# Kernel tuning notes

Measured on AMD Instinct MI355X. Metric: run time of the kernel, lower is better.

The kernel has to match this reference:

```python
import jax, jax.numpy as jnp
import numpy as np

B, T = 64, 2000
Q_DIM, MEM_DIM, ATT_DIM = 1024, 512, 128
N_FILTERS, KERNEL = 32, 31


def setup_inputs() -> dict:
    key = jax.random.key(0)
    ks = jax.random.split(key, 8)
    s = lambda fan_in: 1.0 / np.sqrt(fan_in)
    return {
        "attention_hidden_state": jax.random.normal(ks[0], (B, Q_DIM), jnp.float32),
        "memory": jax.random.normal(ks[1], (B, T, MEM_DIM), jnp.float32),
        "attention_weights_cat": jax.random.uniform(ks[2], (B, 2, T), jnp.float32),
        "W_query": jax.random.normal(ks[3], (Q_DIM, ATT_DIM), jnp.float32) * s(Q_DIM),
        "W_memory": jax.random.normal(ks[4], (MEM_DIM, ATT_DIM), jnp.float32) * s(MEM_DIM),
        "W_v": jax.random.normal(ks[5], (ATT_DIM, 1), jnp.float32) * s(ATT_DIM),
        "W_conv": jax.random.normal(ks[6], (KERNEL, 2, N_FILTERS), jnp.float32) * s(KERNEL * 2),  # WIO layout
        "W_loc": jax.random.normal(ks[7], (N_FILTERS, ATT_DIM), jnp.float32) * s(N_FILTERS),
    }


def reference(attention_hidden_state, memory, attention_weights_cat,
              W_query, W_memory, W_v, W_conv, W_loc):
    # processed query: [B, 1, D]
    pq = jnp.tanh(attention_hidden_state @ W_query)[:, None, :]
    # processed memory: [B, T, D]
    pm = jnp.tanh(jnp.einsum('btm,md->btd', memory, W_memory))
    # location features: Conv1D 'same', no bias, channels-last input [B, T, 2]
    awc = jnp.transpose(attention_weights_cat, (0, 2, 1))
    conv = jax.lax.conv_general_dilated(
        awc, W_conv, window_strides=(1,), padding='SAME',
        dimension_numbers=('NWC', 'WIO', 'NWC'))  # [B, T, F]
    ploc = jnp.tanh(conv @ W_loc)  # [B, T, D]
    # energies: [B, T]
    energies = jnp.squeeze(jnp.tanh(pq + ploc + pm) @ W_v, -1)
    attention_weights = jax.nn.softmax(energies, axis=1)  # [B, T]
    attention_context = jnp.einsum('bt,btm->bm', attention_weights, memory)
    return attention_context, attention_weights
```

## Files before the change

### kernel.cpp

```cpp
#include <hip/hip_runtime.h>
#include <hip/hip_bf16.h>

typedef __attribute__((ext_vector_type(8))) short s16x8;
typedef __attribute__((ext_vector_type(4))) float f32x4;

#define B_SZ 64
#define T_SZ 2000
#define QD 1024
#define MD 512
#define AD 128
#define NF 32
#define KW 31
#define NTILE 63
#define ASTRIDE 1056

__device__ __forceinline__ unsigned short f2bf(float f) {
    unsigned int u = __float_as_uint(f);
    unsigned int r = (u + 0x7FFFu + ((u >> 16) & 1u)) >> 16;
    return (unsigned short)r;
}
__device__ __forceinline__ unsigned int pack2bf_manual(float a, float b) {
    return (unsigned int)f2bf(a) | ((unsigned int)f2bf(b) << 16);
}
__device__ __forceinline__ unsigned int pack2bf(float a, float b) {
    union { __hip_bfloat162 h; unsigned int u; } cv;
    cv.h = __float22bfloat162_rn(float2{a, b});
    return cv.u;
}
__device__ __forceinline__ float fast_tanh(float x) {
    float ax = fabsf(x);
    float e = __expf(2.0f * ax);
    float r = 1.0f - 2.0f * __builtin_amdgcn_rcpf(e + 1.0f);
    return x < 0.0f ? -r : r;
}

__global__ __launch_bounds__(512) void prep_kernel(
    const float* __restrict__ ahs, const float* __restrict__ Wq,
    const float* __restrict__ Wm, const float* __restrict__ Wl,
    float* __restrict__ pq, unsigned short* __restrict__ WB,
    unsigned short* __restrict__ WL) {
    const int blk = blockIdx.x, tid = threadIdx.x;
    if (blk < 64) {
        __shared__ float q_sm[QD];
        __shared__ float part[3][AD];
        ((float2*)q_sm)[tid] = ((const float2*)(ahs + blk * QD))[tid];
        __syncthreads();
        const int d = tid & 127, kh = tid >> 7;
        const int k0 = kh * 256;
        float a0 = 0, a1 = 0, a2 = 0, a3 = 0;
        #pragma unroll 4
        for (int k = k0; k < k0 + 256; k += 4) {
            a0 += q_sm[k]     * Wq[(k)     * AD + d];
            a1 += q_sm[k + 1] * Wq[(k + 1) * AD + d];
            a2 += q_sm[k + 2] * Wq[(k + 2) * AD + d];
            a3 += q_sm[k + 3] * Wq[(k + 3) * AD + d];
        }
        float s = (a0 + a1) + (a2 + a3);
        if (kh) part[kh - 1][d] = s;
        __syncthreads();
        if (tid < AD)
            pq[blk * AD + tid] =
                fast_tanh((s + part[0][tid]) + (part[1][tid] + part[2][tid]));
    } else if (blk < 80) {
        int cidx = (blk - 64) * 512 + tid;
        int n = cidx >> 10, s = (cidx >> 6) & 15, l = cidx & 63;
        int col = n * 16 + (l & 15);
        int krow = s * 32 + (l >> 4) * 8;
        float v[8];
        #pragma unroll
        for (int j = 0; j < 8; ++j) v[j] = Wm[(krow + j) * AD + col];
        uint4 pk;
        pk.x = pack2bf(v[0], v[1]); pk.y = pack2bf(v[2], v[3]);
        pk.z = pack2bf(v[4], v[5]); pk.w = pack2bf(v[6], v[7]);
        *(uint4*)(WB + cidx * 8) = pk;
    } else {
        int cidx = tid;
        int n = cidx >> 6, l = cidx & 63;
        int col = n * 16 + (l & 15);
        int krow = (l >> 4) * 8;
        float v[8];
        #pragma unroll
        for (int j = 0; j < 8; ++j) v[j] = Wl[(krow + j) * AD + col];
        uint4 pk;
        pk.x = pack2bf_manual(v[0], v[1]); pk.y = pack2bf_manual(v[2], v[3]);
        pk.z = pack2bf_manual(v[4], v[5]); pk.w = pack2bf_manual(v[6], v[7]);
        *(uint4*)(WL + cidx * 8) = pk;
    }
}

__global__ __launch_bounds__(256, 4) void energy_kernel(
    const float* __restrict__ memory, const float* __restrict__ awcat,
    const float* __restrict__ Wconv, const float* __restrict__ Wv,
    const float* __restrict__ pq, const unsigned short* __restrict__ WB,
    const unsigned short* __restrict__ WL, float* __restrict__ wts,
    float* __restrict__ ctile, float* __restrict__ mloc,
    float* __restrict__ Stile) {
    const int tile = blockIdx.x;
    const int b = blockIdx.y;
    const int t0 = tile * 32;
    const int tid = threadIdx.x;

    __shared__ __align__(16) unsigned short Atile[32 * (ASTRIDE / 2)];
    __shared__ float aw_sm[2][64];
    __shared__ __align__(16) unsigned short conv_sm[32 * 40];
    __shared__ float e_part[32][4];
    __shared__ float p_sm[32];

    float4 v[16];
    {
        const float4* msrc = (const float4*)(memory + ((size_t)b * T_SZ + t0) * MD);
        const bool full = (t0 + 32 <= T_SZ);
        if (full) {
            #pragma unroll
            for (int it = 0; it < 8; ++it) {
                int cid = it * 256 + tid;
                int r = cid >> 6, cc = cid & 63;
                v[2 * it]     = msrc[r * 128 + cc * 2];
                v[2 * it + 1] = msrc[r * 128 + cc * 2 + 1];
            }
        } else {
            #pragma unroll
            for (int it = 0; it < 8; ++it) {
                int cid = it * 256 + tid;
                int r = cid >> 6, cc = cid & 63;
                float4 z = {0, 0, 0, 0};
                bool ok = (t0 + r < T_SZ);
                v[2 * it]     = ok ? msrc[r * 128 + cc * 2]     : z;
                v[2 * it + 1] = ok ? msrc[r * 128 + cc * 2 + 1] : z;
            }
        }
    }

    if (tid < 128) {
        int c = tid >> 6, i = tid & 63;
        float val = 0.0f;
        int tv = t0 - 15 + i;
        if (i < 63 && tv >= 0 && tv < T_SZ) val = awcat[(b * 2 + c) * T_SZ + tv];
        aw_sm[c][i] = val;
    }

    {
        #pragma unroll
        for (int it = 0; it < 8; ++it) {
            int cid = it * 256 + tid;
            int r = cid >> 6, cc = cid & 63;
            float4 v0 = v[2 * it], v1 = v[2 * it + 1];
            uint4 pk;
            pk.x = pack2bf(v0.x, v0.y); pk.y = pack2bf(v0.z, v0.w);
            pk.z = pack2bf(v1.x, v1.y); pk.w = pack2bf(v1.z, v1.w);
            int off = r * ASTRIDE + ((cc * 16) ^ ((r & 7) << 4));
            *(uint4*)((char*)Atile + off) = pk;
        }
    }
    __syncthreads();

    {
        int f = tid & 31, tq = tid >> 5;
        float acc[4] = {0, 0, 0, 0};
        for (int k = 0; k < KW; ++k) {
            #pragma unroll
            for (int c = 0; c < 2; ++c) {
                float wv = Wconv[(k * 2 + c) * NF + f];
                #pragma unroll
                for (int tt = 0; tt < 4; ++tt)
                    acc[tt] += wv * aw_sm[c][tq + tt * 8 + k];
            }
        }
        #pragma unroll
        for (int tt = 0; tt < 4; ++tt)
            conv_sm[(tq + tt * 8) * 40 + f] = f2bf(acc[tt]);
    }
    __syncthreads();

    const int w = tid >> 6, l = tid & 63;
    const int lr = l & 15, lg = l >> 4;
    const int d0 = (2 * w + 0) * 16 + lr;
    const int d1 = (2 * w + 1) * 16 + lr;
    const float pqv0 = pq[b * AD + d0], pqv1 = pq[b * AD + d1];
    const float wvv0 = Wv[d0], wvv1 = Wv[d1];

    f32x4 zero4 = {0, 0, 0, 0};
    f32x4 p00 = zero4, p01 = zero4, p10 = zero4, p11 = zero4;

    const s16x8* wbp = (const s16x8*)WB;
    const int swz = (lr & 7) << 4;
    const int rbase0 = lr * ASTRIDE;
    const int rbase1 = (16 + lr) * ASTRIDE;
    const int inb = lg * 16;

    #pragma unroll
    for (int s = 0; s < 16; ++s) {
        int j = (inb + s * 64) ^ swz;
        s16x8 a0 = *(const s16x8*)((const char*)Atile + rbase0 + j);
        s16x8 a1 = *(const s16x8*)((const char*)Atile + rbase1 + j);
        s16x8 b0 = wbp[((2 * w + 0) * 16 + s) * 64 + l];
        s16x8 b1 = wbp[((2 * w + 1) * 16 + s) * 64 + l];
        p00 = __builtin_amdgcn_mfma_f32_16x16x32_bf16(a0, b0, p00, 0, 0, 0);
        p01 = __builtin_amdgcn_mfma_f32_16x16x32_bf16(a0, b1, p01, 0, 0, 0);
        p10 = __builtin_amdgcn_mfma_f32_16x16x32_bf16(a1, b0, p10, 0, 0, 0);
        p11 = __builtin_amdgcn_mfma_f32_16x16x32_bf16(a1, b1, p11, 0, 0, 0);
    }

    s16x8 la0 = *(const s16x8*)((const char*)conv_sm + (lr * 80 + lg * 16));
    s16x8 la1 = *(const s16x8*)((const char*)conv_sm + ((16 + lr) * 80 + lg * 16));
    const s16x8* wlp = (const s16x8*)WL;
    s16x8 lb0 = wlp[(2 * w + 0) * 64 + l];
    s16x8 lb1 = wlp[(2 * w + 1) * 64 + l];
    f32x4 q00 = __builtin_amdgcn_mfma_f32_16x16x32_bf16(la0, lb0, zero4, 0, 0, 0);
    f32x4 q01 = __builtin_amdgcn_mfma_f32_16x16x32_bf16(la0, lb1, zero4, 0, 0, 0);
    f32x4 q10 = __builtin_amdgcn_mfma_f32_16x16x32_bf16(la1, lb0, zero4, 0, 0, 0);
    f32x4 q11 = __builtin_amdgcn_mfma_f32_16x16x32_bf16(la1, lb1, zero4, 0, 0, 0);

    float vr[8];
    #pragma unroll
    for (int r = 0; r < 4; ++r) {
        vr[r]     = fast_tanh(pqv0 + fast_tanh(q00[r]) + fast_tanh(p00[r])) * wvv0
                  + fast_tanh(pqv1 + fast_tanh(q01[r]) + fast_tanh(p01[r])) * wvv1;
        vr[4 + r] = fast_tanh(pqv0 + fast_tanh(q10[r]) + fast_tanh(p10[r])) * wvv0
                  + fast_tanh(pqv1 + fast_tanh(q11[r]) + fast_tanh(p11[r])) * wvv1;
    }
    #pragma unroll
    for (int j = 0; j < 8; ++j) {
        float vv = vr[j];
        vv += __shfl_xor(vv, 1);
        vv += __shfl_xor(vv, 2);
        vv += __shfl_xor(vv, 4);
        vv += __shfl_xor(vv, 8);
        if (lr == 0) e_part[(j >> 2) * 16 + lg * 4 + (j & 3)][w] = vv;
    }
    __syncthreads();

    if (tid < 32) {
        int t = t0 + tid;
        bool valid = t < T_SZ;
        float e = (e_part[tid][0] + e_part[tid][1]) + (e_part[tid][2] + e_part[tid][3]);
        float m = valid ? e : -3.4e38f;
        m = fmaxf(m, __shfl_xor(m, 1));
        m = fmaxf(m, __shfl_xor(m, 2));
        m = fmaxf(m, __shfl_xor(m, 4));
        m = fmaxf(m, __shfl_xor(m, 8));
        m = fmaxf(m, __shfl_xor(m, 16));
        float p = valid ? __expf(e - m) : 0.0f;
        p_sm[tid] = p;
        float S = p;
        S += __shfl_xor(S, 1);
        S += __shfl_xor(S, 2);
        S += __shfl_xor(S, 4);
        S += __shfl_xor(S, 8);
        S += __shfl_xor(S, 16);
        if (valid) wts[b * T_SZ + t] = p;
        if (tid == 0) { mloc[b * NTILE + tile] = m; Stile[b * NTILE + tile] = S; }
    }
    __syncthreads();

    {
        float c0 = 0.0f, c1 = 0.0f;
        const int boff = tid * 4;
        #pragma unroll
        for (int t = 0; t < 32; ++t) {
            float p = p_sm[t];
            unsigned int pk = *(const unsigned int*)(
                (const char*)Atile + t * ASTRIDE + (boff ^ ((t & 7) << 4)));
            c0 += p * __uint_as_float(pk << 16);
            c1 += p * __uint_as_float(pk & 0xffff0000u);
        }
        float2 o; o.x = c0; o.y = c1;
        ((float2*)ctile)[((b * NTILE + tile) << 8) + tid] = o;
    }
}

__global__ __launch_bounds__(256) void finalize_kernel(
    const float* __restrict__ mloc, const float* __restrict__ Stile,
    const float* __restrict__ ctile, float* __restrict__ wts,
    float* __restrict__ ctx) {
    const int b = blockIdx.x, h = blockIdx.y, tid = threadIdx.x;
    __shared__ float sc_sm[NTILE + 1];
    if (tid < 64) {
        float m = (tid < NTILE) ? mloc[b * NTILE + tid] : -3.4e38f;
        float s = (tid < NTILE) ? Stile[b * NTILE + tid] : 0.0f;
        float M = m;
        M = fmaxf(M, __shfl_xor(M, 1));  M = fmaxf(M, __shfl_xor(M, 2));
        M = fmaxf(M, __shfl_xor(M, 4));  M = fmaxf(M, __shfl_xor(M, 8));
        M = fmaxf(M, __shfl_xor(M, 16)); M = fmaxf(M, __shfl_xor(M, 32));
        float e = __expf(m - M);
        float z = e * s;
        z += __shfl_xor(z, 1);  z += __shfl_xor(z, 2);
        z += __shfl_xor(z, 4);  z += __shfl_xor(z, 8);
        z += __shfl_xor(z, 16); z += __shfl_xor(z, 32);
        if (tid < NTILE) sc_sm[tid] = e / z;
    }
    __syncthreads();

    if (h == 0) {
        #pragma unroll
        for (int i = 0; i < 8; ++i) {
            int idx = tid + i * 256;
            if (idx < T_SZ) wts[b * T_SZ + idx] *= sc_sm[idx >> 5];
        }
    }

    float a = 0.0f;
    const float* cb = ctile + ((size_t)b * NTILE << 9) + h * 256 + tid;
    #pragma unroll 7
    for (int tl = 0; tl < NTILE; ++tl) a += sc_sm[tl] * cb[(size_t)tl << 9];
    ctx[b * MD + h * 256 + tid] = a;
}

extern "C" void kernel_launch(void* const* d_in, const int* in_sizes, int n_in,
                              void* d_out, int out_size, void* d_ws, size_t ws_size,
                              hipStream_t stream) {
    const float* ahs    = (const float*)d_in[0];
    const float* memory = (const float*)d_in[1];
    const float* awcat  = (const float*)d_in[2];
    const float* Wq     = (const float*)d_in[3];
    const float* Wm     = (const float*)d_in[4];
    const float* Wv     = (const float*)d_in[5];
    const float* Wconv  = (const float*)d_in[6];
    const float* Wl     = (const float*)d_in[7];

    float* out = (float*)d_out;
    float* ctx = out;
    float* wts = out + B_SZ * MD;

    char* ws = (char*)d_ws;
    float* pq             = (float*)(ws);
    unsigned short* WB    = (unsigned short*)(ws + 32768);
    unsigned short* WL    = (unsigned short*)(ws + 163840);
    float* mloc           = (float*)(ws + 172032);
    float* Stile          = (float*)(ws + 188160);
    float* ctile          = (float*)(ws + 204800);

    prep_kernel<<<81, 512, 0, stream>>>(ahs, Wq, Wm, Wl, pq, WB, WL);
    energy_kernel<<<dim3(NTILE, B_SZ), 256, 0, stream>>>(
        memory, awcat, Wconv, Wv, pq, WB, WL, wts, ctile, mloc, Stile);
    finalize_kernel<<<dim3(B_SZ, 2), 256, 0, stream>>>(mloc, Stile, ctile, wts, ctx);
}
```

Baseline: 90.54 us.

## Process four tiles per block with register prefetch of the next tile's memory

The energy kernel now loops over four consecutive 32-step tiles per block instead of launching one block per tile, which shrinks the grid from 63 to 16 blocks along T. While the current tile runs its conv, MFMA and context stages, it issues loads into registers for the first half of the next tile's memory rows. This is meant to hide global-load latency behind compute and to amortize the per-block loads of pq and Wv. In exchange it raises register pressure under launch bounds of 4 blocks per CU, which risks spills. It also reduces the number of independent blocks that can hide latency, and adds an extra barrier per tile.

```diff
diff --git a/kernel.cpp b/kernel.cpp
--- a/kernel.cpp
+++ b/kernel.cpp
@@ -88,71 +88,85 @@
     }
 }
 
-__global__ __launch_bounds__(256, 4) void energy_kernel(
+__device__ __forceinline__ void prefetch_half(
+    const float* memory, int b, int tile, int tid, float4 (&v)[8]) {
+    const float4* msrc = (const float4*)(memory + ((size_t)b * T_SZ + tile * 32) * MD);
+    #pragma unroll
+    for (int it = 0; it < 4; ++it) {
+        int cid = it * 256 + tid;
+        int r = cid >> 6, cc = cid & 63;
+        v[2 * it]     = msrc[r * 128 + cc * 2];
+        v[2 * it + 1] = msrc[r * 128 + cc * 2 + 1];
+    }
+}
+
+__device__ __forceinline__ void tile_body(
+    int b, int tile, int tid,
     const float* __restrict__ memory, const float* __restrict__ awcat,
-    const float* __restrict__ Wconv, const float* __restrict__ Wv,
-    const float* __restrict__ pq, const unsigned short* __restrict__ WB,
-    const unsigned short* __restrict__ WL, float* __restrict__ wts,
-    float* __restrict__ ctile, float* __restrict__ mloc,
-    float* __restrict__ Stile) {
-    const int tile = blockIdx.x;
-    const int b = blockIdx.y;
+    const float* __restrict__ Wconv,
+    const unsigned short* __restrict__ WB, const unsigned short* __restrict__ WL,
+    float pqv0, float pqv1, float wvv0, float wvv1,
+    float* __restrict__ wts, float* __restrict__ ctile,
+    float* __restrict__ mloc, float* __restrict__ Stile,
+    unsigned short* Atile, float (*aw_sm)[64], unsigned short* conv_sm,
+    float (*e_part)[4], float* p_sm,
+    float4 (&vin)[8], float4 (&vnext)[8], bool doPref) {
     const int t0 = tile * 32;
-    const int tid = threadIdx.x;
-
-    __shared__ __align__(16) unsigned short Atile[32 * (ASTRIDE / 2)];
-    __shared__ float aw_sm[2][64];
-    __shared__ __align__(16) unsigned short conv_sm[32 * 40];
-    __shared__ float e_part[32][4];
-    __shared__ float p_sm[32];
-
-    float4 v[16];
-    {
-        const float4* msrc = (const float4*)(memory + ((size_t)b * T_SZ + t0) * MD);
-        const bool full = (t0 + 32 <= T_SZ);
-        if (full) {
-            #pragma unroll
-            for (int it = 0; it < 8; ++it) {
-                int cid = it * 256 + tid;
-                int r = cid >> 6, cc = cid & 63;
-                v[2 * it]     = msrc[r * 128 + cc * 2];
-                v[2 * it + 1] = msrc[r * 128 + cc * 2 + 1];
-            }
-        } else {
-            #pragma unroll
-            for (int it = 0; it < 8; ++it) {
-                int cid = it * 256 + tid;
-                int r = cid >> 6, cc = cid & 63;
-                float4 z = {0, 0, 0, 0};
-                bool ok = (t0 + r < T_SZ);
-                v[2 * it]     = ok ? msrc[r * 128 + cc * 2]     : z;
-                v[2 * it + 1] = ok ? msrc[r * 128 + cc * 2 + 1] : z;
-            }
-        }
-    }
-
+    const float4* msrc = (const float4*)(memory + ((size_t)b * T_SZ + t0) * MD);
+    char* Ac = (char*)Atile;
+
+    float4 v2[8];
+    if (t0 + 32 <= T_SZ) {
+        #pragma unroll
+        for (int it = 0; it < 4; ++it) {
+            int cid = it * 256 + tid;
+            int r = 16 + (cid >> 6), cc = cid & 63;
+            v2[2 * it]     = msrc[r * 128 + cc * 2];
+            v2[2 * it + 1] = msrc[r * 128 + cc * 2 + 1];
+        }
+    } else {
+        #pragma unroll
+        for (int it = 0; it < 4; ++it) {
+            int cid = it * 256 + tid;
+            int r = 16 + (cid >> 6), cc = cid & 63;
+            float4 z = {0, 0, 0, 0};
+            bool ok = (t0 + r) < T_SZ;
+            v2[2 * it]     = ok ? msrc[r * 128 + cc * 2]     : z;
+            v2[2 * it + 1] = ok ? msrc[r * 128 + cc * 2 + 1] : z;
+        }
+    }
+
+    float awv = 0.0f;
+    const int awc_c = tid >> 6, awc_i = tid & 63;
     if (tid < 128) {
-        int c = tid >> 6, i = tid & 63;
-        float val = 0.0f;
-        int tv = t0 - 15 + i;
-        if (i < 63 && tv >= 0 && tv < T_SZ) val = awcat[(b * 2 + c) * T_SZ + tv];
-        aw_sm[c][i] = val;
-    }
-
-    {
-        #pragma unroll
-        for (int it = 0; it < 8; ++it) {
-            int cid = it * 256 + tid;
-            int r = cid >> 6, cc = cid & 63;
-            float4 v0 = v[2 * it], v1 = v[2 * it + 1];
-            uint4 pk;
-            pk.x = pack2bf(v0.x, v0.y); pk.y = pack2bf(v0.z, v0.w);
-            pk.z = pack2bf(v1.x, v1.y); pk.w = pack2bf(v1.z, v1.w);
-            int off = r * ASTRIDE + ((cc * 16) ^ ((r & 7) << 4));
-            *(uint4*)((char*)Atile + off) = pk;
-        }
-    }
-    __syncthreads();
+        int tv = t0 - 15 + awc_i;
+        if (awc_i < 63 && tv >= 0 && tv < T_SZ) awv = awcat[(b * 2 + awc_c) * T_SZ + tv];
+    }
+
+    #pragma unroll
+    for (int it = 0; it < 4; ++it) {
+        int cid = it * 256 + tid;
+        int r = cid >> 6, cc = cid & 63;
+        float4 a0 = vin[2 * it], a1 = vin[2 * it + 1];
+        uint4 pk;
+        pk.x = pack2bf(a0.x, a0.y); pk.y = pack2bf(a0.z, a0.w);
+        pk.z = pack2bf(a1.x, a1.y); pk.w = pack2bf(a1.z, a1.w);
+        *(uint4*)(Ac + r * ASTRIDE + ((cc * 16) ^ ((r & 7) << 4))) = pk;
+    }
+    #pragma unroll
+    for (int it = 0; it < 4; ++it) {
+        int cid = it * 256 + tid;
+        int r = 16 + (cid >> 6), cc = cid & 63;
+        float4 a0 = v2[2 * it], a1 = v2[2 * it + 1];
+        uint4 pk;
+        pk.x = pack2bf(a0.x, a0.y); pk.y = pack2bf(a0.z, a0.w);
+        pk.z = pack2bf(a1.x, a1.y); pk.w = pack2bf(a1.z, a1.w);
+        *(uint4*)(Ac + r * ASTRIDE + ((cc * 16) ^ ((r & 7) << 4))) = pk;
+    }
+    if (tid < 128) aw_sm[awc_c][awc_i] = awv;
+    __syncthreads();
+
+    if (doPref) prefetch_half(memory, b, tile + 1, tid, vnext);
 
     {
         int f = tid & 31, tq = tid >> 5;
@@ -174,10 +188,6 @@
 
     const int w = tid >> 6, l = tid & 63;
     const int lr = l & 15, lg = l >> 4;
-    const int d0 = (2 * w + 0) * 16 + lr;
-    const int d1 = (2 * w + 1) * 16 + lr;
-    const float pqv0 = pq[b * AD + d0], pqv1 = pq[b * AD + d1];
-    const float wvv0 = Wv[d0], wvv1 = Wv[d1];
 
     f32x4 zero4 = {0, 0, 0, 0};
     f32x4 p00 = zero4, p01 = zero4, p10 = zero4, p11 = zero4;
@@ -191,8 +201,8 @@
     #pragma unroll
     for (int s = 0; s < 16; ++s) {
         int j = (inb + s * 64) ^ swz;
-        s16x8 a0 = *(const s16x8*)((const char*)Atile + rbase0 + j);
-        s16x8 a1 = *(const s16x8*)((const char*)Atile + rbase1 + j);
+        s16x8 a0 = *(const s16x8*)(Ac + rbase0 + j);
+        s16x8 a1 = *(const s16x8*)(Ac + rbase1 + j);
         s16x8 b0 = wbp[((2 * w + 0) * 16 + s) * 64 + l];
         s16x8 b1 = wbp[((2 * w + 1) * 16 + s) * 64 + l];
         p00 = __builtin_amdgcn_mfma_f32_16x16x32_bf16(a0, b0, p00, 0, 0, 0);
@@ -260,13 +270,59 @@
         for (int t = 0; t < 32; ++t) {
             float p = p_sm[t];
             unsigned int pk = *(const unsigned int*)(
-                (const char*)Atile + t * ASTRIDE + (boff ^ ((t & 7) << 4)));
+                Ac + t * ASTRIDE + (boff ^ ((t & 7) << 4)));
             c0 += p * __uint_as_float(pk << 16);
             c1 += p * __uint_as_float(pk & 0xffff0000u);
         }
         float2 o; o.x = c0; o.y = c1;
         ((float2*)ctile)[((b * NTILE + tile) << 8) + tid] = o;
     }
+    __syncthreads();
+}
+
+__global__ __launch_bounds__(256, 4) void energy_kernel(
+    const float* __restrict__ memory, const float* __restrict__ awcat,
+    const float* __restrict__ Wconv, const float* __restrict__ Wv,
+    const float* __restrict__ pq, const unsigned short* __restrict__ WB,
+    const unsigned short* __restrict__ WL, float* __restrict__ wts,
+    float* __restrict__ ctile, float* __restrict__ mloc,
+    float* __restrict__ Stile) {
+    const int gx = blockIdx.x;
+    const int b = blockIdx.y;
+    const int tbase = gx * 4;
+    const int ntiles = (tbase + 4 <= NTILE) ? 4 : (NTILE - tbase);
+    const int tid = threadIdx.x;
+
+    __shared__ __align__(16) unsigned short Atile[32 * (ASTRIDE / 2)];
+    __shared__ float aw_sm[2][64];
+    __shared__ __align__(16) unsigned short conv_sm[32 * 40];
+    __shared__ float e_part[32][4];
+    __shared__ float p_sm[32];
+
+    const int w = tid >> 6, lr = tid & 15;
+    const int d0 = (2 * w + 0) * 16 + lr;
+    const int d1 = (2 * w + 1) * 16 + lr;
+    const float pqv0 = pq[b * AD + d0], pqv1 = pq[b * AD + d1];
+    const float wvv0 = Wv[d0], wvv1 = Wv[d1];
+
+    float4 vA[8], vB[8];
+    prefetch_half(memory, b, tbase, tid, vA);
+
+    tile_body(b, tbase + 0, tid, memory, awcat, Wconv, WB, WL,
+              pqv0, pqv1, wvv0, wvv1, wts, ctile, mloc, Stile,
+              Atile, aw_sm, conv_sm, e_part, p_sm, vA, vB, ntiles > 1);
+    if (ntiles > 1)
+        tile_body(b, tbase + 1, tid, memory, awcat, Wconv, WB, WL,
+                  pqv0, pqv1, wvv0, wvv1, wts, ctile, mloc, Stile,
+                  Atile, aw_sm, conv_sm, e_part, p_sm, vB, vA, ntiles > 2);
+    if (ntiles > 2)
+        tile_body(b, tbase + 2, tid, memory, awcat, Wconv, WB, WL,
+                  pqv0, pqv1, wvv0, wvv1, wts, ctile, mloc, Stile,
+                  Atile, aw_sm, conv_sm, e_part, p_sm, vA, vB, ntiles > 3);
+    if (ntiles > 3)
+        tile_body(b, tbase + 3, tid, memory, awcat, Wconv, WB, WL,
+                  pqv0, pqv1, wvv0, wvv1, wts, ctile, mloc, Stile,
+                  Atile, aw_sm, conv_sm, e_part, p_sm, vB, vA, false);
 }
 
 __global__ __launch_bounds__(256) void finalize_kernel(
@@ -331,7 +387,7 @@
     float* ctile          = (float*)(ws + 204800);
 
     prep_kernel<<<81, 512, 0, stream>>>(ahs, Wq, Wm, Wl, pq, WB, WL);
-    energy_kernel<<<dim3(NTILE, B_SZ), 256, 0, stream>>>(
+    energy_kernel<<<dim3(16, B_SZ), 256, 0, stream>>>(
         memory, awcat, Wconv, Wv, pq, WB, WL, wts, ctile, mloc, Stile);
     finalize_kernel<<<dim3(B_SZ, 2), 256, 0, stream>>>(mloc, Stile, ctile, wts, ctx);
 }
```

New measurement: 302.4 us. 234% more time.

## Fold conv weights into location projection and compute ploc via im2col MFMA

Applied to the files above, without the earlier changes.

Precomputes the product of the conv weights and W_loc (62x128) in the prep kernel, so the energy kernel builds an im2col tile of attention weights and runs two MFMA k-steps instead of a scalar 31-tap conv plus a separate MFMA. This removes the per-block scalar convolution loop and one barrier. The awcat load is also issued before the memory loads, and the full/partial load branches are merged. The cost is a heavier prep block and a different bf16 rounding point, since the combined weights and the raw attention weights are quantised instead of the conv output.

```diff
diff --git a/kernel.cpp b/kernel.cpp
--- a/kernel.cpp
+++ b/kernel.cpp
@@ -13,14 +13,12 @@
 #define KW 31
 #define NTILE 63
 #define ASTRIDE 1056
+#define APSTRIDE 136
 
 __device__ __forceinline__ unsigned short f2bf(float f) {
     unsigned int u = __float_as_uint(f);
     unsigned int r = (u + 0x7FFFu + ((u >> 16) & 1u)) >> 16;
     return (unsigned short)r;
-}
-__device__ __forceinline__ unsigned int pack2bf_manual(float a, float b) {
-    return (unsigned int)f2bf(a) | ((unsigned int)f2bf(b) << 16);
 }
 __device__ __forceinline__ unsigned int pack2bf(float a, float b) {
     union { __hip_bfloat162 h; unsigned int u; } cv;
@@ -36,9 +34,9 @@
 
 __global__ __launch_bounds__(512) void prep_kernel(
     const float* __restrict__ ahs, const float* __restrict__ Wq,
-    const float* __restrict__ Wm, const float* __restrict__ Wl,
-    float* __restrict__ pq, unsigned short* __restrict__ WB,
-    unsigned short* __restrict__ WL) {
+    const float* __restrict__ Wm, const float* __restrict__ Wconv,
+    const float* __restrict__ Wl, float* __restrict__ pq,
+    unsigned short* __restrict__ WB, unsigned short* __restrict__ W2B) {
     const int blk = blockIdx.x, tid = threadIdx.x;
     if (blk < 64) {
         __shared__ float q_sm[QD];
@@ -74,69 +72,80 @@
         pk.z = pack2bf(v[4], v[5]); pk.w = pack2bf(v[6], v[7]);
         *(uint4*)(WB + cidx * 8) = pk;
     } else {
-        int cidx = tid;
-        int n = cidx >> 6, l = cidx & 63;
-        int col = n * 16 + (l & 15);
-        int krow = (l >> 4) * 8;
-        float v[8];
-        #pragma unroll
-        for (int j = 0; j < 8; ++j) v[j] = Wl[(krow + j) * AD + col];
-        uint4 pk;
-        pk.x = pack2bf_manual(v[0], v[1]); pk.y = pack2bf_manual(v[2], v[3]);
-        pk.z = pack2bf_manual(v[4], v[5]); pk.w = pack2bf_manual(v[6], v[7]);
-        *(uint4*)(WL + cidx * 8) = pk;
+        __shared__ float wl_sm[NF * AD];
+        for (int h = tid; h < NF * AD; h += 512) wl_sm[h] = Wl[h];
+        __syncthreads();
+        #pragma unroll
+        for (int h = 0; h < 16; ++h) {
+            int idx = h * 512 + tid;
+            int j = idx & 7, l = (idx >> 3) & 63, ns = idx >> 9;
+            int s = ns & 1, n = ns >> 1;
+            int lr = l & 15, lg = l >> 4;
+            int kc = 32 * s + 8 * lg + j;
+            int d = 16 * n + lr;
+            float acc = 0.0f;
+            if (kc < 62) {
+                const float* wrow = Wconv + (kc >> 1) * 2 * NF + (kc & 1) * NF;
+                #pragma unroll 8
+                for (int f = 0; f < NF; ++f) acc += wrow[f] * wl_sm[f * AD + d];
+            }
+            W2B[idx] = f2bf(acc);
+        }
     }
 }
 
 __global__ __launch_bounds__(256, 4) void energy_kernel(
     const float* __restrict__ memory, const float* __restrict__ awcat,
-    const float* __restrict__ Wconv, const float* __restrict__ Wv,
-    const float* __restrict__ pq, const unsigned short* __restrict__ WB,
-    const unsigned short* __restrict__ WL, float* __restrict__ wts,
-    float* __restrict__ ctile, float* __restrict__ mloc,
-    float* __restrict__ Stile) {
+    const float* __restrict__ Wv, const float* __restrict__ pq,
+    const unsigned short* __restrict__ WB, const unsigned short* __restrict__ W2B,
+    float* __restrict__ wts, float* __restrict__ ctile,
+    float* __restrict__ mloc, float* __restrict__ Stile) {
     const int tile = blockIdx.x;
     const int b = blockIdx.y;
     const int t0 = tile * 32;
     const int tid = threadIdx.x;
 
     __shared__ __align__(16) unsigned short Atile[32 * (ASTRIDE / 2)];
-    __shared__ float aw_sm[2][64];
-    __shared__ __align__(16) unsigned short conv_sm[32 * 40];
+    __shared__ float aw2[64][2];
+    __shared__ __align__(16) unsigned short Aploc[32 * (APSTRIDE / 2)];
     __shared__ float e_part[32][4];
     __shared__ float p_sm[32];
 
-    float4 v[16];
-    {
-        const float4* msrc = (const float4*)(memory + ((size_t)b * T_SZ + t0) * MD);
-        const bool full = (t0 + 32 <= T_SZ);
-        if (full) {
-            #pragma unroll
-            for (int it = 0; it < 8; ++it) {
-                int cid = it * 256 + tid;
-                int r = cid >> 6, cc = cid & 63;
-                v[2 * it]     = msrc[r * 128 + cc * 2];
-                v[2 * it + 1] = msrc[r * 128 + cc * 2 + 1];
-            }
-        } else {
-            #pragma unroll
-            for (int it = 0; it < 8; ++it) {
-                int cid = it * 256 + tid;
-                int r = cid >> 6, cc = cid & 63;
-                float4 z = {0, 0, 0, 0};
-                bool ok = (t0 + r < T_SZ);
-                v[2 * it]     = ok ? msrc[r * 128 + cc * 2]     : z;
-                v[2 * it + 1] = ok ? msrc[r * 128 + cc * 2 + 1] : z;
-            }
-        }
-    }
-
+    float awv = 0.0f;
     if (tid < 128) {
         int c = tid >> 6, i = tid & 63;
-        float val = 0.0f;
         int tv = t0 - 15 + i;
-        if (i < 63 && tv >= 0 && tv < T_SZ) val = awcat[(b * 2 + c) * T_SZ + tv];
-        aw_sm[c][i] = val;
+        if (i < 63 && tv >= 0 && tv < T_SZ) awv = awcat[(b * 2 + c) * T_SZ + tv];
+    }
+
+    float4 v[16];
+    {
+        const float4* msrc = (const float4*)(memory + ((size_t)b * T_SZ + t0) * MD);
+        #pragma unroll
+        for (int it = 0; it < 8; ++it) {
+            int cid = it * 256 + tid;
+            int r = cid >> 6, cc = cid & 63;
+            float4 z = {0, 0, 0, 0};
+            bool ok = (t0 + r < T_SZ);
+            v[2 * it]     = ok ? msrc[r * 128 + cc * 2]     : z;
+            v[2 * it + 1] = ok ? msrc[r * 128 + cc * 2 + 1] : z;
+        }
+    }
+
+    if (tid < 128) aw2[tid & 63][tid >> 6] = awv;
+    __syncthreads();
+
+    {
+        int row = tid >> 3, ch = tid & 7;
+        uint4 pk;
+        unsigned int* pw = (unsigned int*)&pk;
+        #pragma unroll
+        for (int jj = 0; jj < 4; ++jj) {
+            int k = ch * 4 + jj;
+            float2 x = (k < 31) ? *(const float2*)aw2[row + k] : float2{0.0f, 0.0f};
+            pw[jj] = pack2bf(x.x, x.y);
+        }
+        *(uint4*)((char*)Aploc + row * APSTRIDE + ch * 16) = pk;
     }
 
     {
@@ -154,24 +163,6 @@
     }
     __syncthreads();
 
-    {
-        int f = tid & 31, tq = tid >> 5;
-        float acc[4] = {0, 0, 0, 0};
-        for (int k = 0; k < KW; ++k) {
-            #pragma unroll
-            for (int c = 0; c < 2; ++c) {
-                float wv = Wconv[(k * 2 + c) * NF + f];
-                #pragma unroll
-                for (int tt = 0; tt < 4; ++tt)
-                    acc[tt] += wv * aw_sm[c][tq + tt * 8 + k];
-            }
-        }
-        #pragma unroll
-        for (int tt = 0; tt < 4; ++tt)
-            conv_sm[(tq + tt * 8) * 40 + f] = f2bf(acc[tt]);
-    }
-    __syncthreads();
-
     const int w = tid >> 6, l = tid & 63;
     const int lr = l & 15, lg = l >> 4;
     const int d0 = (2 * w + 0) * 16 + lr;
@@ -187,12 +178,13 @@
     const int rbase0 = lr * ASTRIDE;
     const int rbase1 = (16 + lr) * ASTRIDE;
     const int inb = lg * 16;
+    const char* Ac = (const char*)Atile;
 
     #pragma unroll
     for (int s = 0; s < 16; ++s) {
         int j = (inb + s * 64) ^ swz;
-        s16x8 a0 = *(const s16x8*)((const char*)Atile + rbase0 + j);
-        s16x8 a1 = *(const s16x8*)((const char*)Atile + rbase1 + j);
+        s16x8 a0 = *(const s16x8*)(Ac + rbase0 + j);
+        s16x8 a1 = *(const s16x8*)(Ac + rbase1 + j);
         s16x8 b0 = wbp[((2 * w + 0) * 16 + s) * 64 + l];
         s16x8 b1 = wbp[((2 * w + 1) * 16 + s) * 64 + l];
         p00 = __builtin_amdgcn_mfma_f32_16x16x32_bf16(a0, b0, p00, 0, 0, 0);
@@ -201,15 +193,22 @@
         p11 = __builtin_amdgcn_mfma_f32_16x16x32_bf16(a1, b1, p11, 0, 0, 0);
     }
 
-    s16x8 la0 = *(const s16x8*)((const char*)conv_sm + (lr * 80 + lg * 16));
-    s16x8 la1 = *(const s16x8*)((const char*)conv_sm + ((16 + lr) * 80 + lg * 16));
-    const s16x8* wlp = (const s16x8*)WL;
-    s16x8 lb0 = wlp[(2 * w + 0) * 64 + l];
-    s16x8 lb1 = wlp[(2 * w + 1) * 64 + l];
-    f32x4 q00 = __builtin_amdgcn_mfma_f32_16x16x32_bf16(la0, lb0, zero4, 0, 0, 0);
-    f32x4 q01 = __builtin_amdgcn_mfma_f32_16x16x32_bf16(la0, lb1, zero4, 0, 0, 0);
-    f32x4 q10 = __builtin_amdgcn_mfma_f32_16x16x32_bf16(la1, lb0, zero4, 0, 0, 0);
-    f32x4 q11 = __builtin_amdgcn_mfma_f32_16x16x32_bf16(la1, lb1, zero4, 0, 0, 0);
+    f32x4 q00 = zero4, q01 = zero4, q10 = zero4, q11 = zero4;
+    {
+        const s16x8* w2p = (const s16x8*)W2B;
+        const char* Apc = (const char*)Aploc;
+        #pragma unroll
+        for (int s = 0; s < 2; ++s) {
+            s16x8 a0 = *(const s16x8*)(Apc + lr * APSTRIDE + inb + s * 64);
+            s16x8 a1 = *(const s16x8*)(Apc + (16 + lr) * APSTRIDE + inb + s * 64);
+            s16x8 b0 = w2p[(((2 * w + 0) * 2 + s) * 64) + l];
+            s16x8 b1 = w2p[(((2 * w + 1) * 2 + s) * 64) + l];
+            q00 = __builtin_amdgcn_mfma_f32_16x16x32_bf16(a0, b0, q00, 0, 0, 0);
+            q01 = __builtin_amdgcn_mfma_f32_16x16x32_bf16(a0, b1, q01, 0, 0, 0);
+            q10 = __builtin_amdgcn_mfma_f32_16x16x32_bf16(a1, b0, q10, 0, 0, 0);
+            q11 = __builtin_amdgcn_mfma_f32_16x16x32_bf16(a1, b1, q11, 0, 0, 0);
+        }
+    }
 
     float vr[8];
     #pragma unroll
@@ -260,7 +259,7 @@
         for (int t = 0; t < 32; ++t) {
             float p = p_sm[t];
             unsigned int pk = *(const unsigned int*)(
-                (const char*)Atile + t * ASTRIDE + (boff ^ ((t & 7) << 4)));
+                Ac + t * ASTRIDE + (boff ^ ((t & 7) << 4)));
             c0 += p * __uint_as_float(pk << 16);
             c1 += p * __uint_as_float(pk & 0xffff0000u);
         }
@@ -325,13 +324,13 @@
     char* ws = (char*)d_ws;
     float* pq             = (float*)(ws);
     unsigned short* WB    = (unsigned short*)(ws + 32768);
-    unsigned short* WL    = (unsigned short*)(ws + 163840);
-    float* mloc           = (float*)(ws + 172032);
-    float* Stile          = (float*)(ws + 188160);
-    float* ctile          = (float*)(ws + 204800);
-
-    prep_kernel<<<81, 512, 0, stream>>>(ahs, Wq, Wm, Wl, pq, WB, WL);
+    unsigned short* W2B   = (unsigned short*)(ws + 163840);
+    float* mloc           = (float*)(ws + 180224);
+    float* Stile          = (float*)(ws + 196608);
+    float* ctile          = (float*)(ws + 221184);
+
+    prep_kernel<<<81, 512, 0, stream>>>(ahs, Wq, Wm, Wconv, Wl, pq, WB, W2B);
     energy_kernel<<<dim3(NTILE, B_SZ), 256, 0, stream>>>(
-        memory, awcat, Wconv, Wv, pq, WB, WL, wts, ctile, mloc, Stile);
+        memory, awcat, Wv, pq, WB, W2B, wts, ctile, mloc, Stile);
     finalize_kernel<<<dim3(B_SZ, 2), 256, 0, stream>>>(mloc, Stile, ctile, wts, ctx);
 }
```

Result: slower. 112.6 us (+24.4%).

## Process two T-tiles per block, prefetching second tile's memory during first tile's compute

Applied to the files above, without the earlier changes.

Each energy block now handles two consecutive 32-row tiles instead of one, halving the grid. The global loads of the second tile's memory rows and attention weights are issued into registers while the first tile's MFMA, tanh and softmax work runs, so load latency overlaps compute. The cost is fewer blocks (less parallelism and tail balance), higher register pressure from holding the prefetched tile, and extra barriers.

```diff
diff --git a/kernel.cpp b/kernel.cpp
--- a/kernel.cpp
+++ b/kernel.cpp
@@ -95,10 +95,12 @@
     const unsigned short* __restrict__ WL, float* __restrict__ wts,
     float* __restrict__ ctile, float* __restrict__ mloc,
     float* __restrict__ Stile) {
-    const int tile = blockIdx.x;
+    const int gx = blockIdx.x;
     const int b = blockIdx.y;
-    const int t0 = tile * 32;
     const int tid = threadIdx.x;
+    const int tile0 = gx * 2;
+    const int t0 = tile0 * 32;
+    const bool two = (gx < 31);
 
     __shared__ __align__(16) unsigned short Atile[32 * (ASTRIDE / 2)];
     __shared__ float aw_sm[2][64];
@@ -106,11 +108,32 @@
     __shared__ float e_part[32][4];
     __shared__ float p_sm[32];
 
+    const int w = tid >> 6, l = tid & 63;
+    const int lr = l & 15, lg = l >> 4;
+    const int d0 = (2 * w + 0) * 16 + lr;
+    const int d1 = (2 * w + 1) * 16 + lr;
+    const float pqv0 = pq[b * AD + d0], pqv1 = pq[b * AD + d1];
+    const float wvv0 = Wv[d0], wvv1 = Wv[d1];
+
+    const s16x8* wbp = (const s16x8*)WB;
+    const s16x8* wlp = (const s16x8*)WL;
+    const int swz = (lr & 7) << 4;
+    const int rbase0 = lr * ASTRIDE;
+    const int rbase1 = (16 + lr) * ASTRIDE;
+    const int inb = lg * 16;
+    const char* Ac = (const char*)Atile;
+    f32x4 zero4 = {0, 0, 0, 0};
+
+    float aw0 = 0.0f;
+    if (tid < 128) {
+        int c = tid >> 6, i = tid & 63;
+        int tv = t0 - 15 + i;
+        if (i < 63 && tv >= 0 && tv < T_SZ) aw0 = awcat[(b * 2 + c) * T_SZ + tv];
+    }
     float4 v[16];
     {
         const float4* msrc = (const float4*)(memory + ((size_t)b * T_SZ + t0) * MD);
-        const bool full = (t0 + 32 <= T_SZ);
-        if (full) {
+        if (two) {
             #pragma unroll
             for (int it = 0; it < 8; ++it) {
                 int cid = it * 256 + tid;
@@ -130,28 +153,18 @@
             }
         }
     }
-
-    if (tid < 128) {
-        int c = tid >> 6, i = tid & 63;
-        float val = 0.0f;
-        int tv = t0 - 15 + i;
-        if (i < 63 && tv >= 0 && tv < T_SZ) val = awcat[(b * 2 + c) * T_SZ + tv];
-        aw_sm[c][i] = val;
-    }
-
-    {
-        #pragma unroll
-        for (int it = 0; it < 8; ++it) {
-            int cid = it * 256 + tid;
-            int r = cid >> 6, cc = cid & 63;
-            float4 v0 = v[2 * it], v1 = v[2 * it + 1];
-            uint4 pk;
-            pk.x = pack2bf(v0.x, v0.y); pk.y = pack2bf(v0.z, v0.w);
-            pk.z = pack2bf(v1.x, v1.y); pk.w = pack2bf(v1.z, v1.w);
-            int off = r * ASTRIDE + ((cc * 16) ^ ((r & 7) << 4));
-            *(uint4*)((char*)Atile + off) = pk;
-        }
-    }
+    #pragma unroll
+    for (int it = 0; it < 8; ++it) {
+        int cid = it * 256 + tid;
+        int r = cid >> 6, cc = cid & 63;
+        uint4 pk;
+        pk.x = pack2bf(v[2 * it].x, v[2 * it].y);
+        pk.y = pack2bf(v[2 * it].z, v[2 * it].w);
+        pk.z = pack2bf(v[2 * it + 1].x, v[2 * it + 1].y);
+        pk.w = pack2bf(v[2 * it + 1].z, v[2 * it + 1].w);
+        *(uint4*)((char*)Atile + r * ASTRIDE + ((cc * 16) ^ ((r & 7) << 4))) = pk;
+    }
+    if (tid < 128) aw_sm[tid >> 6][tid & 63] = aw0;
     __syncthreads();
 
     {
@@ -172,27 +185,12 @@
     }
     __syncthreads();
 
-    const int w = tid >> 6, l = tid & 63;
-    const int lr = l & 15, lg = l >> 4;
-    const int d0 = (2 * w + 0) * 16 + lr;
-    const int d1 = (2 * w + 1) * 16 + lr;
-    const float pqv0 = pq[b * AD + d0], pqv1 = pq[b * AD + d1];
-    const float wvv0 = Wv[d0], wvv1 = Wv[d1];
-
-    f32x4 zero4 = {0, 0, 0, 0};
     f32x4 p00 = zero4, p01 = zero4, p10 = zero4, p11 = zero4;
-
-    const s16x8* wbp = (const s16x8*)WB;
-    const int swz = (lr & 7) << 4;
-    const int rbase0 = lr * ASTRIDE;
-    const int rbase1 = (16 + lr) * ASTRIDE;
-    const int inb = lg * 16;
-
     #pragma unroll
     for (int s = 0; s < 16; ++s) {
         int j = (inb + s * 64) ^ swz;
-        s16x8 a0 = *(const s16x8*)((const char*)Atile + rbase0 + j);
-        s16x8 a1 = *(const s16x8*)((const char*)Atile + rbase1 + j);
+        s16x8 a0 = *(const s16x8*)(Ac + rbase0 + j);
+        s16x8 a1 = *(const s16x8*)(Ac + rbase1 + j);
         s16x8 b0 = wbp[((2 * w + 0) * 16 + s) * 64 + l];
         s16x8 b1 = wbp[((2 * w + 1) * 16 + s) * 64 + l];
         p00 = __builtin_amdgcn_mfma_f32_16x16x32_bf16(a0, b0, p00, 0, 0, 0);
@@ -201,32 +199,50 @@
         p11 = __builtin_amdgcn_mfma_f32_16x16x32_bf16(a1, b1, p11, 0, 0, 0);
     }
 
-    s16x8 la0 = *(const s16x8*)((const char*)conv_sm + (lr * 80 + lg * 16));
-    s16x8 la1 = *(const s16x8*)((const char*)conv_sm + ((16 + lr) * 80 + lg * 16));
-    const s16x8* wlp = (const s16x8*)WL;
-    s16x8 lb0 = wlp[(2 * w + 0) * 64 + l];
-    s16x8 lb1 = wlp[(2 * w + 1) * 64 + l];
-    f32x4 q00 = __builtin_amdgcn_mfma_f32_16x16x32_bf16(la0, lb0, zero4, 0, 0, 0);
-    f32x4 q01 = __builtin_amdgcn_mfma_f32_16x16x32_bf16(la0, lb1, zero4, 0, 0, 0);
-    f32x4 q10 = __builtin_amdgcn_mfma_f32_16x16x32_bf16(la1, lb0, zero4, 0, 0, 0);
-    f32x4 q11 = __builtin_amdgcn_mfma_f32_16x16x32_bf16(la1, lb1, zero4, 0, 0, 0);
-
-    float vr[8];
-    #pragma unroll
-    for (int r = 0; r < 4; ++r) {
-        vr[r]     = fast_tanh(pqv0 + fast_tanh(q00[r]) + fast_tanh(p00[r])) * wvv0
-                  + fast_tanh(pqv1 + fast_tanh(q01[r]) + fast_tanh(p01[r])) * wvv1;
-        vr[4 + r] = fast_tanh(pqv0 + fast_tanh(q10[r]) + fast_tanh(p10[r])) * wvv0
-                  + fast_tanh(pqv1 + fast_tanh(q11[r]) + fast_tanh(p11[r])) * wvv1;
-    }
-    #pragma unroll
-    for (int j = 0; j < 8; ++j) {
-        float vv = vr[j];
-        vv += __shfl_xor(vv, 1);
-        vv += __shfl_xor(vv, 2);
-        vv += __shfl_xor(vv, 4);
-        vv += __shfl_xor(vv, 8);
-        if (lr == 0) e_part[(j >> 2) * 16 + lg * 4 + (j & 3)][w] = vv;
+    float aw1 = 0.0f;
+    if (two) {
+        const float4* msrc1 =
+            (const float4*)(memory + ((size_t)b * T_SZ + t0 + 32) * MD);
+        #pragma unroll
+        for (int it = 0; it < 8; ++it) {
+            int cid = it * 256 + tid;
+            int r = cid >> 6, cc = cid & 63;
+            v[2 * it]     = msrc1[r * 128 + cc * 2];
+            v[2 * it + 1] = msrc1[r * 128 + cc * 2 + 1];
+        }
+        if (tid < 128) {
+            int c = tid >> 6, i = tid & 63;
+            if (i < 63) aw1 = awcat[(b * 2 + c) * T_SZ + (t0 + 17 + i)];
+        }
+    }
+
+    {
+        s16x8 la0 = *(const s16x8*)((const char*)conv_sm + (lr * 80 + lg * 16));
+        s16x8 la1 = *(const s16x8*)((const char*)conv_sm + ((16 + lr) * 80 + lg * 16));
+        s16x8 lb0 = wlp[(2 * w + 0) * 64 + l];
+        s16x8 lb1 = wlp[(2 * w + 1) * 64 + l];
+        f32x4 q00 = __builtin_amdgcn_mfma_f32_16x16x32_bf16(la0, lb0, zero4, 0, 0, 0);
+        f32x4 q01 = __builtin_amdgcn_mfma_f32_16x16x32_bf16(la0, lb1, zero4, 0, 0, 0);
+        f32x4 q10 = __builtin_amdgcn_mfma_f32_16x16x32_bf16(la1, lb0, zero4, 0, 0, 0);
+        f32x4 q11 = __builtin_amdgcn_mfma_f32_16x16x32_bf16(la1, lb1, zero4, 0, 0, 0);
+
+        float vr[8];
+        #pragma unroll
+        for (int r = 0; r < 4; ++r) {
+            vr[r]     = fast_tanh(pqv0 + fast_tanh(q00[r]) + fast_tanh(p00[r])) * wvv0
+                      + fast_tanh(pqv1 + fast_tanh(q01[r]) + fast_tanh(p01[r])) * wvv1;
+            vr[4 + r] = fast_tanh(pqv0 + fast_tanh(q10[r]) + fast_tanh(p10[r])) * wvv0
+                      + fast_tanh(pqv1 + fast_tanh(q11[r]) + fast_tanh(p11[r])) * wvv1;
+        }
+        #pragma unroll
+        for (int j = 0; j < 8; ++j) {
+            float vv = vr[j];
+            vv += __shfl_xor(vv, 1);
+            vv += __shfl_xor(vv, 2);
+            vv += __shfl_xor(vv, 4);
+            vv += __shfl_xor(vv, 8);
+            if (lr == 0) e_part[(j >> 2) * 16 + lg * 4 + (j & 3)][w] = vv;
+        }
     }
     __syncthreads();
 
@@ -249,7 +265,7 @@
         S += __shfl_xor(S, 8);
         S += __shfl_xor(S, 16);
         if (valid) wts[b * T_SZ + t] = p;
-        if (tid == 0) { mloc[b * NTILE + tile] = m; Stile[b * NTILE + tile] = S; }
+        if (tid == 0) { mloc[b * NTILE + tile0] = m; Stile[b * NTILE + tile0] = S; }
     }
     __syncthreads();
 
@@ -260,12 +276,129 @@
         for (int t = 0; t < 32; ++t) {
             float p = p_sm[t];
             unsigned int pk = *(const unsigned int*)(
-                (const char*)Atile + t * ASTRIDE + (boff ^ ((t & 7) << 4)));
+                Ac + t * ASTRIDE + (boff ^ ((t & 7) << 4)));
             c0 += p * __uint_as_float(pk << 16);
             c1 += p * __uint_as_float(pk & 0xffff0000u);
         }
         float2 o; o.x = c0; o.y = c1;
-        ((float2*)ctile)[((b * NTILE + tile) << 8) + tid] = o;
+        ((float2*)ctile)[((b * NTILE + tile0) << 8) + tid] = o;
+    }
+
+    if (!two) return;
+    __syncthreads();
+
+    #pragma unroll
+    for (int it = 0; it < 8; ++it) {
+        int cid = it * 256 + tid;
+        int r = cid >> 6, cc = cid & 63;
+        uint4 pk;
+        pk.x = pack2bf(v[2 * it].x, v[2 * it].y);
+        pk.y = pack2bf(v[2 * it].z, v[2 * it].w);
+        pk.z = pack2bf(v[2 * it + 1].x, v[2 * it + 1].y);
+        pk.w = pack2bf(v[2 * it + 1].z, v[2 * it + 1].w);
+        *(uint4*)((char*)Atile + r * ASTRIDE + ((cc * 16) ^ ((r & 7) << 4))) = pk;
+    }
+    if (tid < 128) aw_sm[tid >> 6][tid & 63] = aw1;
+    __syncthreads();
+
+    {
+        int f = tid & 31, tq = tid >> 5;
+        float acc[4] = {0, 0, 0, 0};
+        for (int k = 0; k < KW; ++k) {
+            #pragma unroll
+            for (int c = 0; c < 2; ++c) {
+                float wv = Wconv[(k * 2 + c) * NF + f];
+                #pragma unroll
+                for (int tt = 0; tt < 4; ++tt)
+                    acc[tt] += wv * aw_sm[c][tq + tt * 8 + k];
+            }
+        }
+        #pragma unroll
+        for (int tt = 0; tt < 4; ++tt)
+            conv_sm[(tq + tt * 8) * 40 + f] = f2bf(acc[tt]);
+    }
+    __syncthreads();
+
+    {
+        f32x4 s00 = zero4, s01 = zero4, s10 = zero4, s11 = zero4;
+        #pragma unroll
+        for (int s = 0; s < 16; ++s) {
+            int j = (inb + s * 64) ^ swz;
+            s16x8 a0 = *(const s16x8*)(Ac + rbase0 + j);
+            s16x8 a1 = *(const s16x8*)(Ac + rbase1 + j);
+            s16x8 b0 = wbp[((2 * w + 0) * 16 + s) * 64 + l];
+            s16x8 b1 = wbp[((2 * w + 1) * 16 + s) * 64 + l];
+            s00 = __builtin_amdgcn_mfma_f32_16x16x32_bf16(a0, b0, s00, 0, 0, 0);
+            s01 = __builtin_amdgcn_mfma_f32_16x16x32_bf16(a0, b1, s01, 0, 0, 0);
+            s10 = __builtin_amdgcn_mfma_f32_16x16x32_bf16(a1, b0, s10, 0, 0, 0);
+            s11 = __builtin_amdgcn_mfma_f32_16x16x32_bf16(a1, b1, s11, 0, 0, 0);
+        }
+        s16x8 la0 = *(const s16x8*)((const char*)conv_sm + (lr * 80 + lg * 16));
+        s16x8 la1 = *(const s16x8*)((const char*)conv_sm + ((16 + lr) * 80 + lg * 16));
+        s16x8 lb0 = wlp[(2 * w + 0) * 64 + l];
+        s16x8 lb1 = wlp[(2 * w + 1) * 64 + l];
+        f32x4 q00 = __builtin_amdgcn_mfma_f32_16x16x32_bf16(la0, lb0, zero4, 0, 0, 0);
+        f32x4 q01 = __builtin_amdgcn_mfma_f32_16x16x32_bf16(la0, lb1, zero4, 0, 0, 0);
+        f32x4 q10 = __builtin_amdgcn_mfma_f32_16x16x32_bf16(la1, lb0, zero4, 0, 0, 0);
+        f32x4 q11 = __builtin_amdgcn_mfma_f32_16x16x32_bf16(la1, lb1, zero4, 0, 0, 0);
+
+        float vr[8];
+        #pragma unroll
+        for (int r = 0; r < 4; ++r) {
+            vr[r]     = fast_tanh(pqv0 + fast_tanh(q00[r]) + fast_tanh(s00[r])) * wvv0
+                      + fast_tanh(pqv1 + fast_tanh(q01[r]) + fast_tanh(s01[r])) * wvv1;
+            vr[4 + r] = fast_tanh(pqv0 + fast_tanh(q10[r]) + fast_tanh(s10[r])) * wvv0
+                      + fast_tanh(pqv1 + fast_tanh(q11[r]) + fast_tanh(s11[r])) * wvv1;
+        }
+        #pragma unroll
+        for (int j = 0; j < 8; ++j) {
+            float vv = vr[j];
+            vv += __shfl_xor(vv, 1);
+            vv += __shfl_xor(vv, 2);
+            vv += __shfl_xor(vv, 4);
+            vv += __shfl_xor(vv, 8);
+            if (lr == 0) e_part[(j >> 2) * 16 + lg * 4 + (j & 3)][w] = vv;
+        }
+    }
+    __syncthreads();
+
+    if (tid < 32) {
+        float e = (e_part[tid][0] + e_part[tid][1]) + (e_part[tid][2] + e_part[tid][3]);
+        float m = e;
+        m = fmaxf(m, __shfl_xor(m, 1));
+        m = fmaxf(m, __shfl_xor(m, 2));
+        m = fmaxf(m, __shfl_xor(m, 4));
+        m = fmaxf(m, __shfl_xor(m, 8));
+        m = fmaxf(m, __shfl_xor(m, 16));
+        float p = __expf(e - m);
+        p_sm[tid] = p;
+        float S = p;
+        S += __shfl_xor(S, 1);
+        S += __shfl_xor(S, 2);
+        S += __shfl_xor(S, 4);
+        S += __shfl_xor(S, 8);
+        S += __shfl_xor(S, 16);
+        wts[b * T_SZ + t0 + 32 + tid] = p;
+        if (tid == 0) {
+            mloc[b * NTILE + tile0 + 1] = m;
+            Stile[b * NTILE + tile0 + 1] = S;
+        }
+    }
+    __syncthreads();
+
+    {
+        float c0 = 0.0f, c1 = 0.0f;
+        const int boff = tid * 4;
+        #pragma unroll
+        for (int t = 0; t < 32; ++t) {
+            float p = p_sm[t];
+            unsigned int pk = *(const unsigned int*)(
+                Ac + t * ASTRIDE + (boff ^ ((t & 7) << 4)));
+            c0 += p * __uint_as_float(pk << 16);
+            c1 += p * __uint_as_float(pk & 0xffff0000u);
+        }
+        float2 o; o.x = c0; o.y = c1;
+        ((float2*)ctile)[((b * NTILE + tile0 + 1) << 8) + tid] = o;
     }
 }
 
@@ -331,7 +464,7 @@
     float* ctile          = (float*)(ws + 204800);
 
     prep_kernel<<<81, 512, 0, stream>>>(ahs, Wq, Wm, Wl, pq, WB, WL);
-    energy_kernel<<<dim3(NTILE, B_SZ), 256, 0, stream>>>(
+    energy_kernel<<<dim3(32, B_SZ), 256, 0, stream>>>(
         memory, awcat, Wconv, Wv, pq, WB, WL, wts, ctile, mloc, Stile);
     finalize_kernel<<<dim3(B_SZ, 2), 256, 0, stream>>>(mloc, Stile, ctile, wts, ctx);
 }
```

Measured after the change: 308.7 us. +240.9%, slower.
